# Performance work log

Measured on AMD Instinct MI355X. Metric: run time of the kernel, lower is better.

## Reference

```python
import jax, jax.numpy as jnp
import numpy as np

N_NODES = 10000
N_EDGES = 320000
IN_CH = 128
HID = 64
HEADS = 8
OUT_CH = 2
NEG_SLOPE = 0.2  # PyG GATConv default
EPS = 1e-16      # PyG softmax denominator eps


def setup_inputs() -> dict:
    key = jax.random.key(0)
    ks = jax.random.split(key, 12)
    x = jax.random.normal(ks[0], (N_NODES, IN_CH), dtype=jnp.float32)
    edge_index = jax.random.randint(ks[1], (2, N_EDGES), 0, N_NODES, dtype=jnp.int64)
    s = 0.05
    W1 = jax.random.normal(ks[2], (IN_CH, HEADS * HID), dtype=jnp.float32) * s
    a_src1 = jax.random.normal(ks[3], (HEADS, HID), dtype=jnp.float32) * s
    a_dst1 = jax.random.normal(ks[4], (HEADS, HID), dtype=jnp.float32) * s
    b1 = jnp.zeros((HEADS * HID,), dtype=jnp.float32)
    W2 = jax.random.normal(ks[5], (HEADS * HID, HID), dtype=jnp.float32) * s
    a_src2 = jax.random.normal(ks[6], (1, HID), dtype=jnp.float32) * s
    a_dst2 = jax.random.normal(ks[7], (1, HID), dtype=jnp.float32) * s
    b2 = jnp.zeros((HID,), dtype=jnp.float32)
    Wc = jax.random.normal(ks[8], (HID, OUT_CH), dtype=jnp.float32) * s
    bc = jnp.zeros((OUT_CH,), dtype=jnp.float32)
    return dict(x=x, edge_index=edge_index, W1=W1, a_src1=a_src1, a_dst1=a_dst1,
                b1=b1, W2=W2, a_src2=a_src2, a_dst2=a_dst2, b2=b2, Wc=Wc, bc=bc)


def gat_layer(x, src, dst, W, a_src, a_dst, bias, heads, ch, concat):
    # x: [N, F_in]; src/dst: [E] (self-loops already appended)
    N = x.shape[0]
    h = (x @ W).reshape(N, heads, ch)                 # [N, H, C]
    e_src = jnp.einsum('nhc,hc->nh', h, a_src)        # [N, H]
    e_dst = jnp.einsum('nhc,hc->nh', h, a_dst)
    e = jax.nn.leaky_relu(e_src[src] + e_dst[dst], NEG_SLOPE)  # [E, H]
    # segment softmax over destination nodes (max-shift has zero gradient)
    m = jax.lax.stop_gradient(jax.ops.segment_max(e, dst, num_segments=N))
    w = jnp.exp(e - m[dst])
    denom = jax.ops.segment_sum(w, dst, num_segments=N)
    alpha = w / (denom[dst] + EPS)                    # [E, H]
    # scatter-aggregate weighted source features
    out = jax.ops.segment_sum(h[src] * alpha[:, :, None], dst, num_segments=N)  # [N,H,C]
    out = out.reshape(N, heads * ch) if concat else out.mean(axis=1)
    return out + bias


def reference(x, edge_index, W1, a_src1, a_dst1, b1, W2, a_src2, a_dst2, b2, Wc, bc):
    N = x.shape[0]
    loop = jnp.arange(N, dtype=edge_index.dtype)
    src = jnp.concatenate([edge_index[0], loop])  # PyG add_self_loops=True
    dst = jnp.concatenate([edge_index[1], loop])
    h1 = gat_layer(x, src, dst, W1, a_src1, a_dst1, b1, HEADS, HID, True)
    h1 = jax.nn.elu(h1)
    # dropout is identity in eval mode
    h2 = gat_layer(h1, src, dst, W2, a_src2, a_dst2, b2, 1, HID, False)
    return h2 @ Wc + bc  # [N, 2]
```

## Files before the change

### kernel.cpp

```cpp
#include <hip/hip_runtime.h>
#include <hip/hip_bf16.h>

#define N_NODES 10000
#define N_EDGES 320000
#define IN_CH 128
#define HID 64
#define HEADS 8
#define OUT_CH 2
#define BM 64
#define BK 16
#define BCAP 128
#define MPAD 10048

typedef __attribute__((ext_vector_type(8))) short frag8;
typedef __attribute__((ext_vector_type(4))) float f32x4;

__device__ __forceinline__ unsigned short f2bf(float f) {
    union { float f; unsigned u; } v; v.f = f;
    unsigned r = (v.u + 0x7FFFu + ((v.u >> 16) & 1u)) >> 16;
    return (unsigned short)r;
}

__device__ __forceinline__ void g2l16(const void* g, void* l) {
    __builtin_amdgcn_global_load_lds(
        (__attribute__((address_space(1))) unsigned int*)g,
        (__attribute__((address_space(3))) unsigned int*)l, 16, 0, 0);
}

__global__ __launch_bounds__(256) void prep_split(
    const float* __restrict__ x, const float* __restrict__ W1,
    const float* __restrict__ W2,
    unsigned short* __restrict__ xh, unsigned short* __restrict__ xl,
    unsigned short* __restrict__ w1h, unsigned short* __restrict__ w1l,
    unsigned short* __restrict__ w2h, unsigned short* __restrict__ w2l,
    int* __restrict__ cursor) {
    int bx = blockIdx.x, tid = threadIdx.x;
    if (bx < 628) {
        int idx = bx * 256 + tid;
        int row = idx >> 4, c = idx & 15;
        float f[8];
        if (row < N_NODES) {
            float4 v0 = *(const float4*)&x[(size_t)row * IN_CH + c * 8];
            float4 v1 = *(const float4*)&x[(size_t)row * IN_CH + c * 8 + 4];
            f[0] = v0.x; f[1] = v0.y; f[2] = v0.z; f[3] = v0.w;
            f[4] = v1.x; f[5] = v1.y; f[6] = v1.z; f[7] = v1.w;
        } else {
            #pragma unroll
            for (int j = 0; j < 8; j++) f[j] = 0.f;
        }
        unsigned short hb[8], lb[8];
        #pragma unroll
        for (int j = 0; j < 8; j++) {
            hb[j] = f2bf(f[j]);
            float hf = __uint_as_float((unsigned)hb[j] << 16);
            lb[j] = f2bf(f[j] - hf);
        }
        size_t o = ((size_t)row * 16 + (c ^ (row & 15))) * 8;
        *(ushort4*)&xh[o]     = make_ushort4(hb[0], hb[1], hb[2], hb[3]);
        *(ushort4*)&xh[o + 4] = make_ushort4(hb[4], hb[5], hb[6], hb[7]);
        *(ushort4*)&xl[o]     = make_ushort4(lb[0], lb[1], lb[2], lb[3]);
        *(ushort4*)&xl[o + 4] = make_ushort4(lb[4], lb[5], lb[6], lb[7]);
    } else if (bx < 660) {
        int idx = (bx - 628) * 256 + tid;
        int kb = idx >> 9, c = idx & 511;
        int hh = c >> 6, cc = c & 63;
        unsigned short hb[8], lb[8];
        #pragma unroll
        for (int i = 0; i < 8; i++) {
            float v = W1[(size_t)(kb * 8 + i) * (HEADS * HID) + c];
            hb[i] = f2bf(v);
            float hf = __uint_as_float((unsigned)hb[i] << 16);
            lb[i] = f2bf(v - hf);
        }
        size_t o = (((size_t)hh * 16 + kb) * 64 + cc) * 8;
        *(ushort4*)&w1h[o]     = make_ushort4(hb[0], hb[1], hb[2], hb[3]);
        *(ushort4*)&w1h[o + 4] = make_ushort4(hb[4], hb[5], hb[6], hb[7]);
        *(ushort4*)&w1l[o]     = make_ushort4(lb[0], lb[1], lb[2], lb[3]);
        *(ushort4*)&w1l[o + 4] = make_ushort4(lb[4], lb[5], lb[6], lb[7]);
    } else if (bx < 676) {
        int idx = (bx - 660) * 256 + tid;
        int kb = idx >> 6, c = idx & 63;
        unsigned short hb[8], lb[8];
        #pragma unroll
        for (int i = 0; i < 8; i++) {
            float v = W2[(size_t)(kb * 8 + i) * 64 + c];
            hb[i] = f2bf(v);
            float hf = __uint_as_float((unsigned)hb[i] << 16);
            lb[i] = f2bf(v - hf);
        }
        size_t o = ((size_t)kb * 64 + c) * 8;
        *(ushort4*)&w2h[o]     = make_ushort4(hb[0], hb[1], hb[2], hb[3]);
        *(ushort4*)&w2h[o + 4] = make_ushort4(hb[4], hb[5], hb[6], hb[7]);
        *(ushort4*)&w2l[o]     = make_ushort4(lb[0], lb[1], lb[2], lb[3]);
        *(ushort4*)&w2l[o + 4] = make_ushort4(lb[4], lb[5], lb[6], lb[7]);
    } else {
        int idx = (bx - 676) * 256 + tid;
        if (idx < 2500) *(int4*)&cursor[idx * 4] = make_int4(0, 0, 0, 0);
    }
}

__global__ __launch_bounds__(256) void gemm1_mfma(
    const unsigned short* __restrict__ xh, const unsigned short* __restrict__ xl,
    const unsigned short* __restrict__ w1h, const unsigned short* __restrict__ w1l,
    const float* __restrict__ a_src1, const float* __restrict__ a_dst1,
    unsigned short* __restrict__ hfeatP,
    float* __restrict__ esAll, float* __restrict__ edAll, int M) {
    __shared__ alignas(16) unsigned short Ah[8192];
    __shared__ alignas(16) unsigned short Al[8192];
    __shared__ alignas(16) unsigned short Bh[8192];
    __shared__ alignas(16) unsigned short Bl[8192];
    int tid = threadIdx.x;
    int lane = tid & 63, w = tid >> 6;
    int vb = (blockIdx.x & 7) * 157 + (blockIdx.x >> 3);
    int h  = vb & 7;
    int bm = (vb >> 3) * BM;

    {
        const unsigned short* gAh = xh  + (size_t)bm * 128;
        const unsigned short* gAl = xl  + (size_t)bm * 128;
        const unsigned short* gBh = w1h + (size_t)h * 8192;
        const unsigned short* gBl = w1l + (size_t)h * 8192;
        #pragma unroll
        for (int i = 0; i < 4; i++) {
            int s = w * 4 + i;
            int go = s * 512 + lane * 8;
            g2l16(gAh + go, &Ah[s * 512]);
            g2l16(gAl + go, &Al[s * 512]);
            g2l16(gBh + go, &Bh[s * 512]);
            g2l16(gBl + go, &Bl[s * 512]);
        }
    }
    __syncthreads();

    int col = lane & 15, g4 = lane >> 4;
    int arow = w * 16 + col;
    f32x4 acc[4] = {};
    #pragma unroll
    for (int ks = 0; ks < 4; ks++) {
        int ai = (arow * 16 + ((ks * 4 + g4) ^ col)) * 8;
        frag8 ah = *(const frag8*)&Ah[ai];
        frag8 al = *(const frag8*)&Al[ai];
        #pragma unroll
        for (int ct = 0; ct < 4; ct++) {
            int bi = ((ks * 4 + g4) * 64 + ct * 16 + col) * 8;
            frag8 bhv = *(const frag8*)&Bh[bi];
            frag8 blv = *(const frag8*)&Bl[bi];
            acc[ct] = __builtin_amdgcn_mfma_f32_16x16x32_bf16(ah, bhv, acc[ct], 0, 0, 0);
            acc[ct] = __builtin_amdgcn_mfma_f32_16x16x32_bf16(al, bhv, acc[ct], 0, 0, 0);
            acc[ct] = __builtin_amdgcn_mfma_f32_16x16x32_bf16(ah, blv, acc[ct], 0, 0, 0);
        }
    }

    float asv[4], adv[4];
    #pragma unroll
    for (int ct = 0; ct < 4; ct++) {
        asv[ct] = a_src1[h * 64 + ct * 16 + col];
        adv[ct] = a_dst1[h * 64 + ct * 16 + col];
    }
    #pragma unroll
    for (int r = 0; r < 4; r++) {
        float s = 0.f, d = 0.f;
        #pragma unroll
        for (int ct = 0; ct < 4; ct++) {
            s += acc[ct][r] * asv[ct];
            d += acc[ct][r] * adv[ct];
        }
        #pragma unroll
        for (int off = 1; off < 16; off <<= 1) {
            s += __shfl_xor(s, off, 64);
            d += __shfl_xor(d, off, 64);
        }
        if (col == 0) {
            int gr = bm + w * 16 + g4 * 4 + r;
            if (gr < M) {
                esAll[(size_t)h * M + gr] = s;
                edAll[(size_t)h * M + gr] = d;
            }
        }
    }

    __syncthreads();
    unsigned short* Tr = Ah;
    int wrow = w * 16 + g4 * 4;
    #pragma unroll
    for (int ct = 0; ct < 4; ct++)
        #pragma unroll
        for (int r = 0; r < 4; r++)
            Tr[(wrow + r) * 68 + ct * 16 + col] = f2bf(acc[ct][r]);
    __syncthreads();
    int row = tid >> 2, q = tid & 3;
    int gr = bm + row;
    if (gr < M) {
        int tb = row * 68 + q * 16;
        ushort4 t0 = *(const ushort4*)&Tr[tb];
        ushort4 t1 = *(const ushort4*)&Tr[tb + 4];
        ushort4 t2 = *(const ushort4*)&Tr[tb + 8];
        ushort4 t3 = *(const ushort4*)&Tr[tb + 12];
        unsigned short* dst =
            &hfeatP[(((size_t)(h >> 1) * M + gr) * 128) + (h & 1) * 64 + q * 16];
        *(ushort4*)&dst[0]  = t0;
        *(ushort4*)&dst[4]  = t1;
        *(ushort4*)&dst[8]  = t2;
        *(ushort4*)&dst[12] = t3;
    }
}

__global__ void fill_bucket(const int* __restrict__ src,
                            const int* __restrict__ dst, int E,
                            int* cursor, int* __restrict__ bucket) {
    int i = blockIdx.x * blockDim.x + threadIdx.x;
    if (i < E) {
        int d = dst[i];
        int pos = atomicAdd(&cursor[d], 1);
        bucket[(d << 7) + min(pos, BCAP - 1)] = src[i];
    }
}

__global__ __launch_bounds__(256) void gemm2_mfma(
    const unsigned short* __restrict__ h1h, const unsigned short* __restrict__ h1l,
    const unsigned short* __restrict__ w2h, const unsigned short* __restrict__ w2l,
    const float* __restrict__ a_src2, const float* __restrict__ a_dst2,
    float* __restrict__ hfeat2, float* __restrict__ es2, float* __restrict__ ed2,
    int M) {
    __shared__ alignas(16) unsigned short Ah[8192];
    __shared__ alignas(16) unsigned short Al[8192];
    __shared__ alignas(16) unsigned short Bh[8192];
    __shared__ alignas(16) unsigned short Bl[8192];
    int tid = threadIdx.x;
    int lane = tid & 63, w = tid >> 6;
    int bm = blockIdx.x * 64;
    int col = lane & 15, g4 = lane >> 4;
    int arow = w * 16 + col;

    f32x4 acc[4] = {};
    for (int t = 0; t < 4; t++) {
        #pragma unroll
        for (int i = 0; i < 4; i++) {
            int s = w * 4 + i;
            int lrow = s * 4 + (lane >> 4);
            int cc = lane & 15;
            int gc = t * 16 + (cc ^ (lrow & 15));
            size_t goA = ((size_t)(bm + lrow) * 64 + gc) * 8;
            g2l16(h1h + goA, &Ah[s * 512]);
            g2l16(h1l + goA, &Al[s * 512]);
            size_t goB = ((size_t)t * 1024 + s * 64 + lane) * 8;
            g2l16(w2h + goB, &Bh[s * 512]);
            g2l16(w2l + goB, &Bl[s * 512]);
        }
        __syncthreads();
        #pragma unroll
        for (int ks = 0; ks < 4; ks++) {
            int ai = (arow * 16 + ((ks * 4 + g4) ^ col)) * 8;
            frag8 ah = *(const frag8*)&Ah[ai];
            frag8 al = *(const frag8*)&Al[ai];
            #pragma unroll
            for (int ct = 0; ct < 4; ct++) {
                int bi = ((ks * 4 + g4) * 64 + ct * 16 + col) * 8;
                frag8 bhv = *(const frag8*)&Bh[bi];
                frag8 blv = *(const frag8*)&Bl[bi];
                acc[ct] = __builtin_amdgcn_mfma_f32_16x16x32_bf16(ah, bhv, acc[ct], 0, 0, 0);
                acc[ct] = __builtin_amdgcn_mfma_f32_16x16x32_bf16(al, bhv, acc[ct], 0, 0, 0);
                acc[ct] = __builtin_amdgcn_mfma_f32_16x16x32_bf16(ah, blv, acc[ct], 0, 0, 0);
            }
        }
        __syncthreads();
    }

    float asv[4], adv[4];
    #pragma unroll
    for (int ct = 0; ct < 4; ct++) {
        asv[ct] = a_src2[ct * 16 + col];
        adv[ct] = a_dst2[ct * 16 + col];
    }
    #pragma unroll
    for (int r = 0; r < 4; r++) {
        int gr = bm + w * 16 + g4 * 4 + r;
        float s = 0.f, d = 0.f;
        #pragma unroll
        for (int ct = 0; ct < 4; ct++) {
            s += acc[ct][r] * asv[ct];
            d += acc[ct][r] * adv[ct];
        }
        #pragma unroll
        for (int off = 1; off < 16; off <<= 1) {
            s += __shfl_xor(s, off, 64);
            d += __shfl_xor(d, off, 64);
        }
        if (gr < M) {
            #pragma unroll
            for (int ct = 0; ct < 4; ct++)
                hfeat2[(size_t)gr * 64 + ct * 16 + col] = acc[ct][r];
            if (col == 0) { es2[gr] = s; ed2[gr] = d; }
        }
    }
}

__global__ __launch_bounds__(256) void gat_agg_pair(
    const unsigned short* __restrict__ hfeatP, const float* __restrict__ esAll,
    const float* __restrict__ edAll, const int* __restrict__ bucket,
    const int* __restrict__ cursor, const float* __restrict__ b1,
    unsigned short* __restrict__ h1h, unsigned short* __restrict__ h1l, int M) {
    int bx = blockIdx.x;
    int p = (bx & 7) >> 1;
    int nb = ((bx >> 3) << 1) + (bx & 1);
    int n = nb * 4 + (threadIdx.x >> 6);
    int l = threadIdx.x & 63;
    int g = l >> 4;
    int q = l & 15;
    int hq = q >> 3;
    int sub = l & 31;
    int hs = l >> 5;
    int g4 = g << 2;
    int hbaseB = hq << 7;
    const char* hptr = (const char*)hfeatP + (size_t)p * M * 256 + (q << 4);
    const float* esS = esAll + (size_t)(p * 2 + hs) * M;
    float ednS = edAll[(size_t)(p * 2 + hs) * M + n];
    int start = n << 7;
    int deg = min(cursor[n], 96);
    int total = deg + 1;

    float a[8] = {};
    float dloc = 0.f;
    for (int base = 0; base < total; base += 32) {
        int idx = base + sub;
        int sld = bucket[start + idx];
        int sv = (idx < deg) ? sld : n;
        float wgt = 0.f;
        if (idx <= deg) {
            float e = esS[sv] + ednS;
            e = (e > 0.f) ? e : 0.2f * e;
            wgt = __expf(e);
        }
        dloc += wgt;
        int rb = sv << 8;
        int wb = __float_as_int(wgt);
        int cnt = min(32, total - base);
        for (int i = 0; i < cnt; i += 4) {
            int b0 = (i << 2) + g4;
            int rbg = __builtin_amdgcn_ds_bpermute(b0, rb);
            float wg = __int_as_float(
                __builtin_amdgcn_ds_bpermute(b0 + hbaseB, wb));
            const uint4 hv = *(const uint4*)(hptr + rbg);
            a[0] += wg * __uint_as_float(hv.x << 16);
            a[1] += wg * __uint_as_float(hv.x & 0xFFFF0000u);
            a[2] += wg * __uint_as_float(hv.y << 16);
            a[3] += wg * __uint_as_float(hv.y & 0xFFFF0000u);
            a[4] += wg * __uint_as_float(hv.z << 16);
            a[5] += wg * __uint_as_float(hv.z & 0xFFFF0000u);
            a[6] += wg * __uint_as_float(hv.w << 16);
            a[7] += wg * __uint_as_float(hv.w & 0xFFFF0000u);
        }
    }
    #pragma unroll
    for (int off = 16; off; off >>= 1) dloc += __shfl_xor(dloc, off, 64);
    float dother = __shfl_xor(dloc, 32, 64);
    #pragma unroll
    for (int k = 0; k < 8; k++) {
        a[k] += __shfl_xor(a[k], 16, 64);
        a[k] += __shfl_xor(a[k], 32, 64);
    }
    if (g == 0) {
        float d = (hq == 0) ? dloc : dother;
        d += 1e-16f;
        float inv = __builtin_amdgcn_rcpf(d);
        inv = inv * __fmaf_rn(-d, inv, 2.0f);
        const float4 b0v = *(const float4*)&b1[p * 128 + q * 8];
        const float4 b4v = *(const float4*)&b1[p * 128 + q * 8 + 4];
        float vv[8];
        vv[0] = a[0] * inv + b0v.x; vv[1] = a[1] * inv + b0v.y;
        vv[2] = a[2] * inv + b0v.z; vv[3] = a[3] * inv + b0v.w;
        vv[4] = a[4] * inv + b4v.x; vv[5] = a[5] * inv + b4v.y;
        vv[6] = a[6] * inv + b4v.z; vv[7] = a[7] * inv + b4v.w;
        #pragma unroll
        for (int k = 0; k < 8; k++)
            vv[k] = (vv[k] > 0.f) ? vv[k] : (__expf(vv[k]) - 1.f);
        unsigned short hh[8], hl[8];
        #pragma unroll
        for (int k = 0; k < 8; k++) {
            hh[k] = f2bf(vv[k]);
            float hf = __uint_as_float((unsigned)hh[k] << 16);
            hl[k] = f2bf(vv[k] - hf);
        }
        size_t o = ((size_t)n * 64 + p * 16 + q) * 8;
        *(ushort4*)&h1h[o]     = make_ushort4(hh[0], hh[1], hh[2], hh[3]);
        *(ushort4*)&h1h[o + 4] = make_ushort4(hh[4], hh[5], hh[6], hh[7]);
        *(ushort4*)&h1l[o]     = make_ushort4(hl[0], hl[1], hl[2], hl[3]);
        *(ushort4*)&h1l[o + 4] = make_ushort4(hl[4], hl[5], hl[6], hl[7]);
    }
}

__global__ __launch_bounds__(256) void gat_agg2(
    const float* __restrict__ hfeat2, const float* __restrict__ es,
    const float* __restrict__ ed, const int* __restrict__ bucket,
    const int* __restrict__ cursor, const float* __restrict__ b2,
    const float* __restrict__ Wc, const float* __restrict__ bc,
    float* __restrict__ out) {
    int n = blockIdx.x * 4 + (threadIdx.x >> 6);
    int l = threadIdx.x & 63;
    int g = l >> 4;
    int q = l & 15;
    int g4 = g << 2;
    int qoff = q << 4;
    int start = n << 7;
    int deg = min(cursor[n], 96);
    int total = deg + 1;
    float edn = ed[n];

    float ax = 0.f, ay = 0.f, az = 0.f, aw = 0.f;
    float dloc = 0.f;
    for (int base = 0; base < total; base += 64) {
        int cnt = min(64, total - base);
        float wgt = 0.f;
        int sv = n;
        if (l < cnt) {
            int idx = base + l;
            sv = (idx < deg) ? bucket[start + idx] : n;
            float e = es[sv] + edn;
            e = (e > 0.f) ? e : 0.2f * e;
            wgt = __expf(e);
        }
        dloc += wgt;
        int rb = sv << 8;
        int wb = __float_as_int(wgt);
        for (int i = 0; i < cnt; i += 4) {
            int bidx = (i << 2) + g4;
            int rbg = __builtin_amdgcn_ds_bpermute(bidx, rb);
            float wg = __int_as_float(__builtin_amdgcn_ds_bpermute(bidx, wb));
            const float4 hv = *(const float4*)((const char*)hfeat2 + (rbg + qoff));
            ax += wg * hv.x;
            ay += wg * hv.y;
            az += wg * hv.z;
            aw += wg * hv.w;
        }
    }
    float d = dloc;
    #pragma unroll
    for (int off = 32; off; off >>= 1) d += __shfl_down(d, off, 64);
    d = __shfl(d, 0, 64) + 1e-16f;
    float inv = __builtin_amdgcn_rcpf(d);
    inv = inv * __fmaf_rn(-d, inv, 2.0f);
    ax += __shfl_down(ax, 32, 64); ay += __shfl_down(ay, 32, 64);
    az += __shfl_down(az, 32, 64); aw += __shfl_down(aw, 32, 64);
    ax += __shfl_down(ax, 16, 64); ay += __shfl_down(ay, 16, 64);
    az += __shfl_down(az, 16, 64); aw += __shfl_down(aw, 16, 64);
    float p0 = 0.f, p1 = 0.f;
    if (g == 0) {
        const float4 bq = *(const float4*)&b2[q * 4];
        float h0 = ax * inv + bq.x, h1v = ay * inv + bq.y;
        float h2v = az * inv + bq.z, h3 = aw * inv + bq.w;
        const float2* WcV = (const float2*)Wc;
        float2 w0 = WcV[q * 4 + 0], w1 = WcV[q * 4 + 1];
        float2 w2 = WcV[q * 4 + 2], w3 = WcV[q * 4 + 3];
        p0 = h0 * w0.x + h1v * w1.x + h2v * w2.x + h3 * w3.x;
        p1 = h0 * w0.y + h1v * w1.y + h2v * w2.y + h3 * w3.y;
    }
    #pragma unroll
    for (int off = 1; off < 16; off <<= 1) {
        p0 += __shfl_xor(p0, off, 64);
        p1 += __shfl_xor(p1, off, 64);
    }
    if (l == 0) {
        out[n * 2 + 0] = p0 + bc[0];
        out[n * 2 + 1] = p1 + bc[1];
    }
}

extern "C" void kernel_launch(void* const* d_in, const int* in_sizes, int n_in,
                              void* d_out, int out_size, void* d_ws, size_t ws_size,
                              hipStream_t stream) {
    const float* x      = (const float*)d_in[0];
    const int*   eidx   = (const int*)d_in[1];
    const float* W1     = (const float*)d_in[2];
    const float* a_src1 = (const float*)d_in[3];
    const float* a_dst1 = (const float*)d_in[4];
    const float* b1     = (const float*)d_in[5];
    const float* W2     = (const float*)d_in[6];
    const float* a_src2 = (const float*)d_in[7];
    const float* a_dst2 = (const float*)d_in[8];
    const float* b2     = (const float*)d_in[9];
    const float* Wc     = (const float*)d_in[10];
    const float* bc     = (const float*)d_in[11];
    float* out = (float*)d_out;

    const int N = N_NODES, E = N_EDGES;
    const int* esrc = eidx;
    const int* edst = eidx + E;

    size_t off = 0;
    auto alloc = [&](size_t bytes) {
        void* p = (char*)d_ws + off;
        off += (bytes + 255) & ~(size_t)255;
        return p;
    };
    int*   cursor   = (int*)alloc((size_t)N * 4);
    int*   bucket   = (int*)alloc((size_t)N * BCAP * 4);
    unsigned short* hfeatP = (unsigned short*)alloc((size_t)4 * N * 128 * 2);
    unsigned short* h1h = (unsigned short*)alloc((size_t)MPAD * 512 * 2);
    unsigned short* h1l = (unsigned short*)alloc((size_t)MPAD * 512 * 2);
    float* hfeat2   = (float*)alloc((size_t)N * 64 * 4);
    float* esAll    = (float*)alloc((size_t)HEADS * N * 4);
    float* edAll    = (float*)alloc((size_t)HEADS * N * 4);
    float* es2      = (float*)alloc((size_t)N * 4);
    float* ed2      = (float*)alloc((size_t)N * 4);
    unsigned short* xh  = (unsigned short*)alloc((size_t)MPAD * 128 * 2);
    unsigned short* xl  = (unsigned short*)alloc((size_t)MPAD * 128 * 2);
    unsigned short* w1h = (unsigned short*)alloc((size_t)128 * 512 * 2);
    unsigned short* w1l = (unsigned short*)alloc((size_t)128 * 512 * 2);
    unsigned short* w2h = (unsigned short*)alloc((size_t)512 * 64 * 2);
    unsigned short* w2l = (unsigned short*)alloc((size_t)512 * 64 * 2);

    prep_split<<<686, 256, 0, stream>>>(x, W1, W2, xh, xl, w1h, w1l, w2h, w2l,
                                        cursor);
    gemm1_mfma<<<157 * 8, 256, 0, stream>>>(xh, xl, w1h, w1l, a_src1, a_dst1,
                                            hfeatP, esAll, edAll, N);
    fill_bucket<<<(E + 255) / 256, 256, 0, stream>>>(esrc, edst, E, cursor, bucket);
    gat_agg_pair<<<(N / 4) * 4, 256, 0, stream>>>(hfeatP, esAll, edAll,
                                                  bucket, cursor, b1, h1h, h1l, N);
    gemm2_mfma<<<157, 256, 0, stream>>>(h1h, h1l, w2h, w2l, a_src2, a_dst2,
                                        hfeat2, es2, ed2, N);
    gat_agg2<<<(N + 3) / 4, 256, 0, stream>>>(hfeat2, es2, ed2, bucket, cursor,
                                              b2, Wc, bc, out);
}
```

Baseline: 172.5 us.

## Fuse bucket fill into GEMM1 launch and unroll aggregation gather loops

The edge bucketing kernel is merged into the first GEMM kernel as extra leading blocks, so one launch runs both and the atomic scatter can overlap with the MFMA work. The gather loops in both aggregation kernels are unrolled, fully for full 32-edge chunks and by four otherwise, to put more independent loads in flight. The fill blocks carry the GEMM kernel's large LDS allocation even though they do not use it, which may reduce their occupancy. Unrolling raises register pressure.

```diff
diff --git a/kernel.cpp b/kernel.cpp
--- a/kernel.cpp
+++ b/kernel.cpp
@@ -8,9 +8,9 @@
 #define HEADS 8
 #define OUT_CH 2
 #define BM 64
-#define BK 16
 #define BCAP 128
 #define MPAD 10048
+#define FILL_BLKS 1250
 
 typedef __attribute__((ext_vector_type(8))) short frag8;
 typedef __attribute__((ext_vector_type(4))) float f32x4;
@@ -99,19 +99,33 @@
     }
 }
 
-__global__ __launch_bounds__(256) void gemm1_mfma(
+__global__ __launch_bounds__(256) void gemm1_fill(
     const unsigned short* __restrict__ xh, const unsigned short* __restrict__ xl,
     const unsigned short* __restrict__ w1h, const unsigned short* __restrict__ w1l,
     const float* __restrict__ a_src1, const float* __restrict__ a_dst1,
     unsigned short* __restrict__ hfeatP,
-    float* __restrict__ esAll, float* __restrict__ edAll, int M) {
+    float* __restrict__ esAll, float* __restrict__ edAll,
+    const int* __restrict__ esrc, const int* __restrict__ edst,
+    int* cursor, int* __restrict__ bucket, int M) {
     __shared__ alignas(16) unsigned short Ah[8192];
     __shared__ alignas(16) unsigned short Al[8192];
     __shared__ alignas(16) unsigned short Bh[8192];
     __shared__ alignas(16) unsigned short Bl[8192];
     int tid = threadIdx.x;
+
+    if (blockIdx.x < FILL_BLKS) {
+        int i = blockIdx.x * 256 + tid;
+        if (i < N_EDGES) {
+            int d = edst[i];
+            int pos = atomicAdd(&cursor[d], 1);
+            bucket[(d << 7) + min(pos, BCAP - 1)] = esrc[i];
+        }
+        return;
+    }
+
+    int bxe = blockIdx.x - FILL_BLKS;
     int lane = tid & 63, w = tid >> 6;
-    int vb = (blockIdx.x & 7) * 157 + (blockIdx.x >> 3);
+    int vb = (bxe & 7) * 157 + (bxe >> 3);
     int h  = vb & 7;
     int bm = (vb >> 3) * BM;
 
@@ -205,17 +219,6 @@
     }
 }
 
-__global__ void fill_bucket(const int* __restrict__ src,
-                            const int* __restrict__ dst, int E,
-                            int* cursor, int* __restrict__ bucket) {
-    int i = blockIdx.x * blockDim.x + threadIdx.x;
-    if (i < E) {
-        int d = dst[i];
-        int pos = atomicAdd(&cursor[d], 1);
-        bucket[(d << 7) + min(pos, BCAP - 1)] = src[i];
-    }
-}
-
 __global__ __launch_bounds__(256) void gemm2_mfma(
     const unsigned short* __restrict__ h1h, const unsigned short* __restrict__ h1l,
     const unsigned short* __restrict__ w2h, const unsigned short* __restrict__ w2l,
@@ -293,6 +296,22 @@
             if (col == 0) { es2[gr] = s; ed2[gr] = d; }
         }
     }
+}
+
+#define GATH_P(i) {                                                         \
+    int b0 = ((i) << 2) + g4;                                               \
+    int rbg = __builtin_amdgcn_ds_bpermute(b0, rb);                         \
+    float wg = __int_as_float(                                              \
+        __builtin_amdgcn_ds_bpermute(b0 + hbaseB, wb));                     \
+    const uint4 hv = *(const uint4*)(hptr + rbg);                           \
+    a[0] += wg * __uint_as_float(hv.x << 16);                               \
+    a[1] += wg * __uint_as_float(hv.x & 0xFFFF0000u);                       \
+    a[2] += wg * __uint_as_float(hv.y << 16);                               \
+    a[3] += wg * __uint_as_float(hv.y & 0xFFFF0000u);                       \
+    a[4] += wg * __uint_as_float(hv.z << 16);                               \
+    a[5] += wg * __uint_as_float(hv.z & 0xFFFF0000u);                       \
+    a[6] += wg * __uint_as_float(hv.w << 16);                               \
+    a[7] += wg * __uint_as_float(hv.w & 0xFFFF0000u);                       \
 }
 
 __global__ __launch_bounds__(256) void gat_agg_pair(
@@ -335,20 +354,11 @@
         int rb = sv << 8;
         int wb = __float_as_int(wgt);
         int cnt = min(32, total - base);
-        for (int i = 0; i < cnt; i += 4) {
-            int b0 = (i << 2) + g4;
-            int rbg = __builtin_amdgcn_ds_bpermute(b0, rb);
-            float wg = __int_as_float(
-                __builtin_amdgcn_ds_bpermute(b0 + hbaseB, wb));
-            const uint4 hv = *(const uint4*)(hptr + rbg);
-            a[0] += wg * __uint_as_float(hv.x << 16);
-            a[1] += wg * __uint_as_float(hv.x & 0xFFFF0000u);
-            a[2] += wg * __uint_as_float(hv.y << 16);
-            a[3] += wg * __uint_as_float(hv.y & 0xFFFF0000u);
-            a[4] += wg * __uint_as_float(hv.z << 16);
-            a[5] += wg * __uint_as_float(hv.z & 0xFFFF0000u);
-            a[6] += wg * __uint_as_float(hv.w << 16);
-            a[7] += wg * __uint_as_float(hv.w & 0xFFFF0000u);
+        if (cnt == 32) {
+            #pragma unroll
+            for (int i = 0; i < 32; i += 4) GATH_P(i)
+        } else {
+            for (int i = 0; i < cnt; i += 4) GATH_P(i)
         }
     }
     #pragma unroll
@@ -387,6 +397,17 @@
         *(ushort4*)&h1l[o]     = make_ushort4(hl[0], hl[1], hl[2], hl[3]);
         *(ushort4*)&h1l[o + 4] = make_ushort4(hl[4], hl[5], hl[6], hl[7]);
     }
+}
+
+#define GATH_2(i) {                                                         \
+    int bidx = ((i) << 2) + g4;                                             \
+    int rbg = __builtin_amdgcn_ds_bpermute(bidx, rb);                       \
+    float wg = __int_as_float(__builtin_amdgcn_ds_bpermute(bidx, wb));      \
+    const float4 hv = *(const float4*)((const char*)hfeat2 + (rbg + qoff)); \
+    ax += wg * hv.x;                                                        \
+    ay += wg * hv.y;                                                        \
+    az += wg * hv.z;                                                        \
+    aw += wg * hv.w;                                                        \
 }
 
 __global__ __launch_bounds__(256) void gat_agg2(
@@ -422,16 +443,11 @@
         dloc += wgt;
         int rb = sv << 8;
         int wb = __float_as_int(wgt);
-        for (int i = 0; i < cnt; i += 4) {
-            int bidx = (i << 2) + g4;
-            int rbg = __builtin_amdgcn_ds_bpermute(bidx, rb);
-            float wg = __int_as_float(__builtin_amdgcn_ds_bpermute(bidx, wb));
-            const float4 hv = *(const float4*)((const char*)hfeat2 + (rbg + qoff));
-            ax += wg * hv.x;
-            ay += wg * hv.y;
-            az += wg * hv.z;
-            aw += wg * hv.w;
-        }
+        int i = 0;
+        for (; i + 16 <= cnt; i += 16) {
+            GATH_2(i) GATH_2(i + 4) GATH_2(i + 8) GATH_2(i + 12)
+        }
+        for (; i < cnt; i += 4) GATH_2(i)
     }
     float d = dloc;
     #pragma unroll
@@ -511,9 +527,9 @@
 
     prep_split<<<686, 256, 0, stream>>>(x, W1, W2, xh, xl, w1h, w1l, w2h, w2l,
                                         cursor);
-    gemm1_mfma<<<157 * 8, 256, 0, stream>>>(xh, xl, w1h, w1l, a_src1, a_dst1,
-                                            hfeatP, esAll, edAll, N);
-    fill_bucket<<<(E + 255) / 256, 256, 0, stream>>>(esrc, edst, E, cursor, bucket);
+    gemm1_fill<<<FILL_BLKS + 157 * 8, 256, 0, stream>>>(
+        xh, xl, w1h, w1l, a_src1, a_dst1, hfeatP, esAll, edAll,
+        esrc, edst, cursor, bucket, N);
     gat_agg_pair<<<(N / 4) * 4, 256, 0, stream>>>(hfeatP, esAll, edAll,
                                                   bucket, cursor, b1, h1h, h1l, N);
     gemm2_mfma<<<157, 256, 0, stream>>>(h1h, h1l, w2h, w2l, a_src2, a_dst2,
```

Result: slower. 177.3 us (+2.8%).

## Make GAT aggregation kernels persistent and stage edge records in LDS

Applied to the files above, without the earlier changes.

Both aggregation kernels become grid-stride loops over a fixed number of blocks (2048 and 832), so each wavefront handles several destination nodes instead of one. Each wave now writes its per-edge source offsets and softmax weights into a small LDS record array. Lanes then read them back with a single vector LDS load, replacing the two ds_bpermute lane shuffles per gather step. The goal is lower block launch and scheduling overhead and fewer cross-lane ops in the inner gather loop. The cost is less parallelism for latency hiding and a reliance on wave-synchronous LDS ordering with no barrier.

```diff
diff --git a/kernel.cpp b/kernel.cpp
--- a/kernel.cpp
+++ b/kernel.cpp
@@ -8,9 +8,10 @@
 #define HEADS 8
 #define OUT_CH 2
 #define BM 64
-#define BK 16
 #define BCAP 128
 #define MPAD 10048
+#define AGG1_BLKS 2048
+#define AGG2_BLKS 832
 
 typedef __attribute__((ext_vector_type(8))) short frag8;
 typedef __attribute__((ext_vector_type(4))) float f32x4;
@@ -300,92 +301,98 @@
     const float* __restrict__ edAll, const int* __restrict__ bucket,
     const int* __restrict__ cursor, const float* __restrict__ b1,
     unsigned short* __restrict__ h1h, unsigned short* __restrict__ h1l, int M) {
+    __shared__ alignas(16) unsigned rec[4][32][4];
     int bx = blockIdx.x;
     int p = (bx & 7) >> 1;
-    int nb = ((bx >> 3) << 1) + (bx & 1);
-    int n = nb * 4 + (threadIdx.x >> 6);
+    int wid = threadIdx.x >> 6;
+    int wvp = ((((bx >> 3) << 1) | (bx & 1)) << 2) + wid;
     int l = threadIdx.x & 63;
     int g = l >> 4;
     int q = l & 15;
     int hq = q >> 3;
     int sub = l & 31;
     int hs = l >> 5;
-    int g4 = g << 2;
-    int hbaseB = hq << 7;
+    unsigned (*wrec)[4] = rec[wid];
     const char* hptr = (const char*)hfeatP + (size_t)p * M * 256 + (q << 4);
     const float* esS = esAll + (size_t)(p * 2 + hs) * M;
-    float ednS = edAll[(size_t)(p * 2 + hs) * M + n];
-    int start = n << 7;
-    int deg = min(cursor[n], 96);
-    int total = deg + 1;
-
-    float a[8] = {};
-    float dloc = 0.f;
-    for (int base = 0; base < total; base += 32) {
-        int idx = base + sub;
-        int sld = bucket[start + idx];
-        int sv = (idx < deg) ? sld : n;
-        float wgt = 0.f;
-        if (idx <= deg) {
-            float e = esS[sv] + ednS;
-            e = (e > 0.f) ? e : 0.2f * e;
-            wgt = __expf(e);
-        }
-        dloc += wgt;
-        int rb = sv << 8;
-        int wb = __float_as_int(wgt);
-        int cnt = min(32, total - base);
-        for (int i = 0; i < cnt; i += 4) {
-            int b0 = (i << 2) + g4;
-            int rbg = __builtin_amdgcn_ds_bpermute(b0, rb);
-            float wg = __int_as_float(
-                __builtin_amdgcn_ds_bpermute(b0 + hbaseB, wb));
-            const uint4 hv = *(const uint4*)(hptr + rbg);
-            a[0] += wg * __uint_as_float(hv.x << 16);
-            a[1] += wg * __uint_as_float(hv.x & 0xFFFF0000u);
-            a[2] += wg * __uint_as_float(hv.y << 16);
-            a[3] += wg * __uint_as_float(hv.y & 0xFFFF0000u);
-            a[4] += wg * __uint_as_float(hv.z << 16);
-            a[5] += wg * __uint_as_float(hv.z & 0xFFFF0000u);
-            a[6] += wg * __uint_as_float(hv.w << 16);
-            a[7] += wg * __uint_as_float(hv.w & 0xFFFF0000u);
-        }
-    }
-    #pragma unroll
-    for (int off = 16; off; off >>= 1) dloc += __shfl_xor(dloc, off, 64);
-    float dother = __shfl_xor(dloc, 32, 64);
-    #pragma unroll
-    for (int k = 0; k < 8; k++) {
-        a[k] += __shfl_xor(a[k], 16, 64);
-        a[k] += __shfl_xor(a[k], 32, 64);
-    }
-    if (g == 0) {
-        float d = (hq == 0) ? dloc : dother;
-        d += 1e-16f;
-        float inv = __builtin_amdgcn_rcpf(d);
-        inv = inv * __fmaf_rn(-d, inv, 2.0f);
-        const float4 b0v = *(const float4*)&b1[p * 128 + q * 8];
-        const float4 b4v = *(const float4*)&b1[p * 128 + q * 8 + 4];
-        float vv[8];
-        vv[0] = a[0] * inv + b0v.x; vv[1] = a[1] * inv + b0v.y;
-        vv[2] = a[2] * inv + b0v.z; vv[3] = a[3] * inv + b0v.w;
-        vv[4] = a[4] * inv + b4v.x; vv[5] = a[5] * inv + b4v.y;
-        vv[6] = a[6] * inv + b4v.z; vv[7] = a[7] * inv + b4v.w;
-        #pragma unroll
-        for (int k = 0; k < 8; k++)
-            vv[k] = (vv[k] > 0.f) ? vv[k] : (__expf(vv[k]) - 1.f);
-        unsigned short hh[8], hl[8];
+    const float* edS = edAll + (size_t)(p * 2 + hs) * M;
+
+    for (int n = wvp; n < M; n += 2048) {
+        float ednS = edS[n];
+        int start = n << 7;
+        int deg = min(cursor[n], 96);
+        int total = deg + 1;
+
+        float a[8] = {};
+        float dloc = 0.f;
+        for (int base = 0; base < total; base += 32) {
+            int idx = base + sub;
+            int sld = bucket[start + idx];
+            int sv = (idx < deg) ? sld : n;
+            float wgt = 0.f;
+            if (idx <= deg) {
+                float e = esS[sv] + ednS;
+                e = (e > 0.f) ? e : 0.2f * e;
+                wgt = __expf(e);
+            }
+            dloc += wgt;
+            if (hs == 0) {
+                *(uint2*)&wrec[sub][0] =
+                    make_uint2((unsigned)(sv << 8), __float_as_int(wgt));
+            } else {
+                wrec[sub][2] = __float_as_int(wgt);
+            }
+            int cnt = min(32, total - base);
+            for (int i = 0; i < cnt; i += 4) {
+                const uint4 rv = *(const uint4*)&wrec[i + g][0];
+                float wg = __uint_as_float(hq ? rv.z : rv.y);
+                const uint4 hv = *(const uint4*)(hptr + rv.x);
+                a[0] += wg * __uint_as_float(hv.x << 16);
+                a[1] += wg * __uint_as_float(hv.x & 0xFFFF0000u);
+                a[2] += wg * __uint_as_float(hv.y << 16);
+                a[3] += wg * __uint_as_float(hv.y & 0xFFFF0000u);
+                a[4] += wg * __uint_as_float(hv.z << 16);
+                a[5] += wg * __uint_as_float(hv.z & 0xFFFF0000u);
+                a[6] += wg * __uint_as_float(hv.w << 16);
+                a[7] += wg * __uint_as_float(hv.w & 0xFFFF0000u);
+            }
+        }
+        #pragma unroll
+        for (int off = 16; off; off >>= 1) dloc += __shfl_xor(dloc, off, 64);
+        float dother = __shfl_xor(dloc, 32, 64);
         #pragma unroll
         for (int k = 0; k < 8; k++) {
-            hh[k] = f2bf(vv[k]);
-            float hf = __uint_as_float((unsigned)hh[k] << 16);
-            hl[k] = f2bf(vv[k] - hf);
-        }
-        size_t o = ((size_t)n * 64 + p * 16 + q) * 8;
-        *(ushort4*)&h1h[o]     = make_ushort4(hh[0], hh[1], hh[2], hh[3]);
-        *(ushort4*)&h1h[o + 4] = make_ushort4(hh[4], hh[5], hh[6], hh[7]);
-        *(ushort4*)&h1l[o]     = make_ushort4(hl[0], hl[1], hl[2], hl[3]);
-        *(ushort4*)&h1l[o + 4] = make_ushort4(hl[4], hl[5], hl[6], hl[7]);
+            a[k] += __shfl_xor(a[k], 16, 64);
+            a[k] += __shfl_xor(a[k], 32, 64);
+        }
+        if (g == 0) {
+            float d = (hq == 0) ? dloc : dother;
+            d += 1e-16f;
+            float inv = __builtin_amdgcn_rcpf(d);
+            inv = inv * __fmaf_rn(-d, inv, 2.0f);
+            const float4 b0v = *(const float4*)&b1[p * 128 + q * 8];
+            const float4 b4v = *(const float4*)&b1[p * 128 + q * 8 + 4];
+            float vv[8];
+            vv[0] = a[0] * inv + b0v.x; vv[1] = a[1] * inv + b0v.y;
+            vv[2] = a[2] * inv + b0v.z; vv[3] = a[3] * inv + b0v.w;
+            vv[4] = a[4] * inv + b4v.x; vv[5] = a[5] * inv + b4v.y;
+            vv[6] = a[6] * inv + b4v.z; vv[7] = a[7] * inv + b4v.w;
+            #pragma unroll
+            for (int k = 0; k < 8; k++)
+                vv[k] = (vv[k] > 0.f) ? vv[k] : (__expf(vv[k]) - 1.f);
+            unsigned short hh[8], hl[8];
+            #pragma unroll
+            for (int k = 0; k < 8; k++) {
+                hh[k] = f2bf(vv[k]);
+                float hf = __uint_as_float((unsigned)hh[k] << 16);
+                hl[k] = f2bf(vv[k] - hf);
+            }
+            size_t o = ((size_t)n * 64 + p * 16 + q) * 8;
+            *(ushort4*)&h1h[o]     = make_ushort4(hh[0], hh[1], hh[2], hh[3]);
+            *(ushort4*)&h1h[o + 4] = make_ushort4(hh[4], hh[5], hh[6], hh[7]);
+            *(ushort4*)&h1l[o]     = make_ushort4(hl[0], hl[1], hl[2], hl[3]);
+            *(ushort4*)&h1l[o + 4] = make_ushort4(hl[4], hl[5], hl[6], hl[7]);
+        }
     }
 }
 
@@ -395,73 +402,78 @@
     const int* __restrict__ cursor, const float* __restrict__ b2,
     const float* __restrict__ Wc, const float* __restrict__ bc,
     float* __restrict__ out) {
-    int n = blockIdx.x * 4 + (threadIdx.x >> 6);
+    __shared__ alignas(8) unsigned rec2[4][64][2];
+    int wid = threadIdx.x >> 6;
+    int wv = blockIdx.x * 4 + wid;
     int l = threadIdx.x & 63;
     int g = l >> 4;
     int q = l & 15;
-    int g4 = g << 2;
     int qoff = q << 4;
-    int start = n << 7;
-    int deg = min(cursor[n], 96);
-    int total = deg + 1;
-    float edn = ed[n];
-
-    float ax = 0.f, ay = 0.f, az = 0.f, aw = 0.f;
-    float dloc = 0.f;
-    for (int base = 0; base < total; base += 64) {
-        int cnt = min(64, total - base);
-        float wgt = 0.f;
-        int sv = n;
-        if (l < cnt) {
-            int idx = base + l;
-            sv = (idx < deg) ? bucket[start + idx] : n;
-            float e = es[sv] + edn;
-            e = (e > 0.f) ? e : 0.2f * e;
-            wgt = __expf(e);
-        }
-        dloc += wgt;
-        int rb = sv << 8;
-        int wb = __float_as_int(wgt);
-        for (int i = 0; i < cnt; i += 4) {
-            int bidx = (i << 2) + g4;
-            int rbg = __builtin_amdgcn_ds_bpermute(bidx, rb);
-            float wg = __int_as_float(__builtin_amdgcn_ds_bpermute(bidx, wb));
-            const float4 hv = *(const float4*)((const char*)hfeat2 + (rbg + qoff));
-            ax += wg * hv.x;
-            ay += wg * hv.y;
-            az += wg * hv.z;
-            aw += wg * hv.w;
-        }
-    }
-    float d = dloc;
-    #pragma unroll
-    for (int off = 32; off; off >>= 1) d += __shfl_down(d, off, 64);
-    d = __shfl(d, 0, 64) + 1e-16f;
-    float inv = __builtin_amdgcn_rcpf(d);
-    inv = inv * __fmaf_rn(-d, inv, 2.0f);
-    ax += __shfl_down(ax, 32, 64); ay += __shfl_down(ay, 32, 64);
-    az += __shfl_down(az, 32, 64); aw += __shfl_down(aw, 32, 64);
-    ax += __shfl_down(ax, 16, 64); ay += __shfl_down(ay, 16, 64);
-    az += __shfl_down(az, 16, 64); aw += __shfl_down(aw, 16, 64);
-    float p0 = 0.f, p1 = 0.f;
-    if (g == 0) {
-        const float4 bq = *(const float4*)&b2[q * 4];
-        float h0 = ax * inv + bq.x, h1v = ay * inv + bq.y;
-        float h2v = az * inv + bq.z, h3 = aw * inv + bq.w;
-        const float2* WcV = (const float2*)Wc;
-        float2 w0 = WcV[q * 4 + 0], w1 = WcV[q * 4 + 1];
-        float2 w2 = WcV[q * 4 + 2], w3 = WcV[q * 4 + 3];
-        p0 = h0 * w0.x + h1v * w1.x + h2v * w2.x + h3 * w3.x;
-        p1 = h0 * w0.y + h1v * w1.y + h2v * w2.y + h3 * w3.y;
-    }
-    #pragma unroll
-    for (int off = 1; off < 16; off <<= 1) {
-        p0 += __shfl_xor(p0, off, 64);
-        p1 += __shfl_xor(p1, off, 64);
-    }
-    if (l == 0) {
-        out[n * 2 + 0] = p0 + bc[0];
-        out[n * 2 + 1] = p1 + bc[1];
+    unsigned (*wr2)[2] = rec2[wid];
+
+    for (int n = wv; n < N_NODES; n += AGG2_BLKS * 4) {
+        int start = n << 7;
+        int deg = min(cursor[n], 96);
+        int total = deg + 1;
+        float edn = ed[n];
+
+        float ax = 0.f, ay = 0.f, az = 0.f, aw = 0.f;
+        float dloc = 0.f;
+        for (int base = 0; base < total; base += 64) {
+            int cnt = min(64, total - base);
+            float wgt = 0.f;
+            int sv = n;
+            if (l < cnt) {
+                int idx = base + l;
+                sv = (idx < deg) ? bucket[start + idx] : n;
+                float e = es[sv] + edn;
+                e = (e > 0.f) ? e : 0.2f * e;
+                wgt = __expf(e);
+            }
+            dloc += wgt;
+            *(uint2*)&wr2[l][0] =
+                make_uint2((unsigned)(sv << 8), __float_as_int(wgt));
+            for (int i = 0; i < cnt; i += 4) {
+                const uint2 rv = *(const uint2*)&wr2[i + g][0];
+                float wg = __uint_as_float(rv.y);
+                const float4 hv =
+                    *(const float4*)((const char*)hfeat2 + (rv.x + qoff));
+                ax += wg * hv.x;
+                ay += wg * hv.y;
+                az += wg * hv.z;
+                aw += wg * hv.w;
+            }
+        }
+        float d = dloc;
+        #pragma unroll
+        for (int off = 32; off; off >>= 1) d += __shfl_down(d, off, 64);
+        d = __shfl(d, 0, 64) + 1e-16f;
+        float inv = __builtin_amdgcn_rcpf(d);
+        inv = inv * __fmaf_rn(-d, inv, 2.0f);
+        ax += __shfl_down(ax, 32, 64); ay += __shfl_down(ay, 32, 64);
+        az += __shfl_down(az, 32, 64); aw += __shfl_down(aw, 32, 64);
+        ax += __shfl_down(ax, 16, 64); ay += __shfl_down(ay, 16, 64);
+        az += __shfl_down(az, 16, 64); aw += __shfl_down(aw, 16, 64);
+        float p0 = 0.f, p1 = 0.f;
+        if (g == 0) {
+            const float4 bq = *(const float4*)&b2[q * 4];
+            float h0 = ax * inv + bq.x, h1v = ay * inv + bq.y;
+            float h2v = az * inv + bq.z, h3 = aw * inv + bq.w;
+            const float2* WcV = (const float2*)Wc;
+            float2 w0 = WcV[q * 4 + 0], w1 = WcV[q * 4 + 1];
+            float2 w2 = WcV[q * 4 + 2], w3 = WcV[q * 4 + 3];
+            p0 = h0 * w0.x + h1v * w1.x + h2v * w2.x + h3 * w3.x;
+            p1 = h0 * w0.y + h1v * w1.y + h2v * w2.y + h3 * w3.y;
+        }
+        #pragma unroll
+        for (int off = 1; off < 16; off <<= 1) {
+            p0 += __shfl_xor(p0, off, 64);
+            p1 += __shfl_xor(p1, off, 64);
+        }
+        if (l == 0) {
+            out[n * 2 + 0] = p0 + bc[0];
+            out[n * 2 + 1] = p1 + bc[1];
+        }
     }
 }
 
@@ -514,10 +526,10 @@
     gemm1_mfma<<<157 * 8, 256, 0, stream>>>(xh, xl, w1h, w1l, a_src1, a_dst1,
                                             hfeatP, esAll, edAll, N);
     fill_bucket<<<(E + 255) / 256, 256, 0, stream>>>(esrc, edst, E, cursor, bucket);
-    gat_agg_pair<<<(N / 4) * 4, 256, 0, stream>>>(hfeatP, esAll, edAll,
-                                                  bucket, cursor, b1, h1h, h1l, N);
+    gat_agg_pair<<<AGG1_BLKS, 256, 0, stream>>>(hfeatP, esAll, edAll,
+                                                bucket, cursor, b1, h1h, h1l, N);
     gemm2_mfma<<<157, 256, 0, stream>>>(h1h, h1l, w2h, w2l, a_src2, a_dst2,
                                         hfeat2, es2, ed2, N);
-    gat_agg2<<<(N + 3) / 4, 256, 0, stream>>>(hfeat2, es2, ed2, bucket, cursor,
-                                              b2, Wc, bc, out);
-}
+    gat_agg2<<<AGG2_BLKS, 256, 0, stream>>>(hfeat2, es2, ed2, bucket, cursor,
+                                            b2, Wc, bc, out);
+}
```

Result: slower. 178.8 us (+3.7%).
